# Kernel optimization log

Measured on AMD Instinct MI355X. Metric: run time of the kernel, lower is better.

Reference implementation:

```python
import jax
import jax.numpy as jnp
import numpy as np
from jax.scipy.linalg import expm

H = 2048   # hidden_size
R = 1      # low-rank dimension
B = 2048   # batch of independent (h, x) pairs


def _glorot(key, shape):
    return jax.random.uniform(key, shape, minval=-1.0, maxval=1.0) * jnp.sqrt(2.0 / sum(shape))


def setup_inputs() -> dict:
    key = jax.random.key(0)
    k1, k2, k3, k4, k5, k6 = jax.random.split(key, 6)
    return {
        "h": jax.random.normal(k5, (B, H), dtype=jnp.float32),
        "x": jax.random.normal(k6, (B, H), dtype=jnp.float32),
        # a_diag ~ U(-1, 0) * init_scale (10.0): negative real diagonal
        "a_diag": jax.random.uniform(k1, (H,), minval=-1.0, maxval=0.0) * 10.0,
        "p_vec": _glorot(k2, (H, R)),
        "q_vec": _glorot(k3, (H, R)),
        "b_mat": _glorot(k4, (H, H)),
        "delta": jnp.array(0.1, dtype=jnp.float32),
    }


def reference(h, x, a_diag, p_vec, q_vec, b_mat, delta):
    # A = diag(a_diag) + P Q^T  (DPLR structure, materialized dense as in source)
    A = jnp.diag(a_diag) + p_vec @ q_vec.T                       # [H, H]
    # Discretized state matrix: exp(delta * A)
    expA = expm(delta * A)                                       # [H, H]
    # Discretized input matrix: A^{-1} (exp(delta A) - I) B  (pinv as in source)
    A_inv = jnp.linalg.pinv(A)                                   # [H, H]
    B_disc = A_inv @ (expA - jnp.eye(H, dtype=A.dtype)) @ b_mat  # [H, H]
    # Batched recurrence step: A h + B x  for each row of h, x
    return h @ expA.T + x @ B_disc.T                             # [B, H]
```

## Files before the change

### kernel.cpp

```cpp
#include <hip/hip_runtime.h>

#define MAXM 16
#define NL_CAP 256
#define THETA 0.04f
#define SMEM_BYTES 36864

typedef unsigned short u16;
typedef u16 u16x8 __attribute__((ext_vector_type(8)));
typedef u16 u16x4 __attribute__((ext_vector_type(4)));
typedef __bf16 bf16x8 __attribute__((ext_vector_type(8)));
typedef float f32x4 __attribute__((ext_vector_type(4)));


__device__ __forceinline__ u16 f2bf(float f) {
    unsigned u = __float_as_uint(f);
    return (u16)((u + 0x7fffu + ((u >> 16) & 1u)) >> 16);
}

__global__ __launch_bounds__(256)
void conv_k(const float* __restrict__ x, const float* __restrict__ b,
            u16* __restrict__ xb, u16* __restrict__ bb, long nx, long nb)
{
    long i = ((long)blockIdx.x * 256 + threadIdx.x) * 4;
    if (i < nx) {
        float4 v = *(const float4*)&x[i];
        u16x4 o = {f2bf(v.x), f2bf(v.y), f2bf(v.z), f2bf(v.w)};
        *(u16x4*)&xb[i] = o;
    }
    if (i < nb) {
        float4 v = *(const float4*)&b[i];
        u16x4 o = {f2bf(v.x), f2bf(v.y), f2bf(v.z), f2bf(v.w)};
        *(u16x4*)&bb[i] = o;
    }
}


__device__ __forceinline__ double frcp(double den) {
    double r = (double)__builtin_amdgcn_rcpf((float)den);
    return fma(r, fma(-den, r, 1.0), r);
}


__device__ __forceinline__ void gload_lds16(const void* g, void* l) {
    __builtin_amdgcn_global_load_lds(
        (const __attribute__((address_space(1))) unsigned int*)g,
        (__attribute__((address_space(3))) unsigned int*)l, 16, 0, 0);
}

__device__ __forceinline__ void gemm_tile(u16* Al, u16* Bl, int tid, int bx, int by,
                                          const u16* __restrict__ A,
                                          const u16* __restrict__ B,
                                          float* __restrict__ C,
                                          int Ndim, int Kstride, int Klen)
{
    const int bm = by * 128, bn = bx * 128;
    const int wv = tid >> 6, ln = tid & 63;
    const int wr = (wv >> 1) * 64, wc = (wv & 1) * 64;
    const int fr = ln & 15, fk = (ln >> 4) * 8;

    const int r0 = tid >> 2, c0 = (tid & 3) * 8;
    const u16* Ap0 = A + (size_t)(bm + r0) * Kstride + c0;
    const u16* Ap1 = Ap0 + (size_t)64 * Kstride;
    const u16* Bp0 = B + (size_t)(bn + r0) * Kstride + c0;
    const u16* Bp1 = Bp0 + (size_t)64 * Kstride;
    u16* AlW0 = Al + wv * 512;
    u16* AlW1 = Al + 2048 + wv * 512;
    u16* BlW0 = Bl + wv * 512;
    u16* BlW1 = Bl + 2048 + wv * 512;

    f32x4 acc[4][4];
#pragma unroll
    for (int m = 0; m < 4; ++m)
#pragma unroll
        for (int n = 0; n < 4; ++n) acc[m][n] = (f32x4)0.f;

    for (int kk = 0; kk < Klen; kk += 32) {
        __syncthreads();
        gload_lds16(Ap0 + kk, AlW0);
        gload_lds16(Ap1 + kk, AlW1);
        gload_lds16(Bp0 + kk, BlW0);
        gload_lds16(Bp1 + kk, BlW1);
        __syncthreads();
        u16x8 af[4], bf[4];
#pragma unroll
        for (int m = 0; m < 4; ++m)
            af[m] = *(const u16x8*)&Al[(wr + m * 16 + fr) * 32 + fk];
#pragma unroll
        for (int n = 0; n < 4; ++n)
            bf[n] = *(const u16x8*)&Bl[(wc + n * 16 + fr) * 32 + fk];
#pragma unroll
        for (int m = 0; m < 4; ++m)
#pragma unroll
            for (int n = 0; n < 4; ++n)
                acc[m][n] = __builtin_amdgcn_mfma_f32_16x16x32_bf16(
                    __builtin_bit_cast(bf16x8, af[m]),
                    __builtin_bit_cast(bf16x8, bf[n]), acc[m][n], 0, 0, 0);
    }

    const int crow = (ln >> 4) * 4;
#pragma unroll
    for (int m = 0; m < 4; ++m)
#pragma unroll
        for (int n = 0; n < 4; ++n) {
            const size_t base = (size_t)(bm + wr + m * 16 + crow) * Ndim
                              + bn + wc + n * 16 + fr;
#pragma unroll
            for (int j = 0; j < 4; ++j)
                C[base + (size_t)j * Ndim] = acc[m][n][j];
        }
}

__global__ __launch_bounds__(256)
void bgemm_k(const u16* __restrict__ A, const u16* __restrict__ B,
             float* __restrict__ C, int Ndim, int Kdim)
{
    __shared__ __align__(16) unsigned char smem[SMEM_BYTES];
    gemm_tile((u16*)smem, (u16*)smem + 4096, threadIdx.x,
              blockIdx.x, blockIdx.y, A, B, C, Ndim, Kdim, Kdim);
}


__global__ __launch_bounds__(256)
void g_sgemm_k(const float* __restrict__ A, const float* __restrict__ B,
               float* __restrict__ C, int Mdim, int Ndim, int Kdim)
{
    __shared__ __align__(16) float As[16][132];
    __shared__ __align__(16) float Bs[16][68];
    const int tid = threadIdx.x;
    const int tx = tid & 15, ty = tid >> 4;
    const int bn = blockIdx.x * 64, bm = blockIdx.y * 128;
    const int lrA = tid >> 1, lcA = (tid & 1) << 3;
    const int lrB = tid >> 2, lcB = (tid & 3) << 2;
    const float* Aptr = A + (size_t)(bm + lrA) * Kdim + lcA;
    const float* Bptr = B + (size_t)(bn + lrB) * Kdim + lcB;
    float4 a0 = *(const float4*)(Aptr);
    float4 a1 = *(const float4*)(Aptr + 4);
    float4 b0 = *(const float4*)(Bptr);
    float acc[8][4];
#pragma unroll
    for (int i = 0; i < 8; ++i)
#pragma unroll
        for (int j = 0; j < 4; ++j) acc[i][j] = 0.f;
    for (int kk = 0; kk < Kdim; kk += 16) {
        __syncthreads();
        As[lcA + 0][lrA] = a0.x; As[lcA + 1][lrA] = a0.y;
        As[lcA + 2][lrA] = a0.z; As[lcA + 3][lrA] = a0.w;
        As[lcA + 4][lrA] = a1.x; As[lcA + 5][lrA] = a1.y;
        As[lcA + 6][lrA] = a1.z; As[lcA + 7][lrA] = a1.w;
        Bs[lcB + 0][lrB] = b0.x; Bs[lcB + 1][lrB] = b0.y;
        Bs[lcB + 2][lrB] = b0.z; Bs[lcB + 3][lrB] = b0.w;
        __syncthreads();
        if (kk + 16 < Kdim) {
            a0 = *(const float4*)(Aptr + kk + 16);
            a1 = *(const float4*)(Aptr + kk + 20);
            b0 = *(const float4*)(Bptr + kk + 16);
        }
#pragma unroll
        for (int k = 0; k < 16; ++k) {
            const float4 av0 = *(const float4*)&As[k][ty * 8];
            const float4 av1 = *(const float4*)&As[k][ty * 8 + 4];
            const float4 bv  = *(const float4*)&Bs[k][tx * 4];
            const float avf[8] = {av0.x, av0.y, av0.z, av0.w, av1.x, av1.y, av1.z, av1.w};
            const float bvf[4] = {bv.x, bv.y, bv.z, bv.w};
#pragma unroll
            for (int i = 0; i < 8; ++i)
#pragma unroll
                for (int j = 0; j < 4; ++j) acc[i][j] += avf[i] * bvf[j];
        }
    }
#pragma unroll
    for (int i = 0; i < 8; ++i) {
        const int r = bm + ty * 8 + i;
        float4 v = {acc[i][0], acc[i][1], acc[i][2], acc[i][3]};
        *(float4*)&C[(size_t)r * Ndim + bn + tx * 4] = v;
    }
}


__device__ __forceinline__ double wsum(double x) {
#pragma unroll
    for (int m = 32; m; m >>= 1) x += __shfl_xor(x, m, 64);
    return x;
}
__device__ __forceinline__ float wsumf(float x) {
#pragma unroll
    for (int m = 32; m; m >>= 1) x += __shfl_xor(x, m, 64);
    return x;
}

__device__ __forceinline__ int inert(double s11, double s12, double s22,
                                     double dc, double cS)
{
    double b00 = cS - s11, b01 = -1.0 - s12, b11 = -s22;
    double det = b00 * b11 - b01 * b01, tr = b00 + b11;
    int neg = (det > 0.0) ? ((tr < 0.0) ? 2 : 0) : 1;
    return (int)(dc + 0.5) + neg - 1;
}

__device__ __forceinline__ int lane_evalN32(float tf, double td, int n4,
    const float4* l0, const float4* l1, const float4* l2,
    const double* pc, bool poly, double cS,
    double& g11o, double& g12o, double& g22o)
{
    float s11 = 0.f, s12 = 0.f, s22 = 0.f, dc = 0.f;
#pragma unroll 2
    for (int i = 0; i < n4; ++i) {
        const float4 d4 = l0[i], x4 = l1[i], y4 = l2[i];
        const float dd[4] = {d4.x, d4.y, d4.z, d4.w};
        const float xx[4] = {x4.x, x4.y, x4.z, x4.w};
        const float yy[4] = {y4.x, y4.y, y4.z, y4.w};
#pragma unroll
        for (int e = 0; e < 4; ++e) {
            float den = dd[e] - tf;
            float mag = fmaxf(fabsf(den), 1e-30f);
            den = (den < 0.f) ? -mag : mag;
            const float inv = __builtin_amdgcn_rcpf(den);
            s11 = fmaf(xx[e] * xx[e], inv, s11);
            s12 = fmaf(xx[e] * yy[e], inv, s12);
            s22 = fmaf(yy[e] * yy[e], inv, s22);
            if (dd[e] < tf) dc += 1.f;
        }
    }
    double S11 = (double)s11, S12 = (double)s12, S22 = (double)s22;
    if (poly) {
        S11 += pc[0] + td * (pc[3] + td * (pc[6] + td * pc[9]));
        S12 += pc[1] + td * (pc[4] + td * (pc[7] + td * pc[10]));
        S22 += pc[2] + td * (pc[5] + td * (pc[8] + td * pc[11]));
    }
    g11o = S11; g12o = S12; g22o = S22;
    return inert(S11, S12, S22, (double)dc, cS);
}

__device__ void spec256(unsigned char* smem, int tid,
                        const float* __restrict__ av, const float* __restrict__ pv,
                        const float* __restrict__ qv, double* __restrict__ hdr,
                        float* __restrict__ V)
{
    __builtin_amdgcn_s_setprio(1);

    float* sd2 = (float*)smem;
    float* sw1 = sd2 + 2048;
    float* sw2 = sw1 + 2048;
    float* nl0 = sw2 + 2048;
    float* nl1 = nl0 + NL_CAP;
    float* nl2 = nl1 + NL_CAP;
    double* dsh = (double*)(nl2 + NL_CAP);
    int* ish = (int*)(dsh + 192);

    const int lane = tid & 63, wv = tid >> 6;
    const int j0 = tid * 8;

    float d2r[8], w1r[8], w2r[8];
    double cS = 0, n1 = 0, n2 = 0, mx = 0;
#pragma unroll
    for (int h = 0; h < 2; ++h) {
        float4 aa = *(const float4*)&av[j0 + h * 4];
        float4 pp = *(const float4*)&pv[j0 + h * 4];
        float4 qq = *(const float4*)&qv[j0 + h * 4];
        const float a4[4] = {aa.x, aa.y, aa.z, aa.w};
        const float p4[4] = {pp.x, pp.y, pp.z, pp.w};
        const float q4[4] = {qq.x, qq.y, qq.z, qq.w};
#pragma unroll
        for (int e = 0; e < 4; ++e) {
            const int ix = h * 4 + e;
            d2r[ix] = a4[e] * a4[e];
            w1r[ix] = a4[e] * p4[e];
            w2r[ix] = q4[e];
            sd2[j0 + ix] = d2r[ix]; sw1[j0 + ix] = w1r[ix]; sw2[j0 + ix] = w2r[ix];
            cS += (double)p4[e] * p4[e];
            n1 += (double)w1r[ix] * w1r[ix];
            n2 += (double)w2r[ix] * w2r[ix];
            mx = fmax(mx, (double)d2r[ix]);
        }
    }
    cS = wsum(cS); n1 = wsum(n1); n2 = wsum(n2);
#pragma unroll
    for (int m_ = 32; m_; m_ >>= 1) mx = fmax(mx, __shfl_xor(mx, m_, 64));
    __syncthreads();
    if (lane == 0) { dsh[wv] = cS; dsh[4 + wv] = n1; dsh[8 + wv] = n2; dsh[12 + wv] = mx; }
    __syncthreads();
    cS = 0; n1 = 0; n2 = 0; mx = 0;
    for (int w = 0; w < 4; ++w) {
        cS += dsh[w]; n1 += dsh[4 + w]; n2 += dsh[8 + w];
        mx = fmax(mx, dsh[12 + w]);
    }
    __syncthreads();

    double lo = 0.0;
    double hi = mx + 0.5 * (cS + sqrt(cS * cS + 4.0)) * (n1 + n2) + 1.0;
    for (int r = 0; r < 5; ++r) {
        const double td = lo + (hi - lo) * (double)(wv + 1) / 5.0;
        const float tf = (float)td;
        float s11 = 0.f, s12 = 0.f, s22 = 0.f, dc = 0.f;
        for (int i4 = lane; i4 < 512; i4 += 64) {
            const float4 dd = ((const float4*)sd2)[i4];
            const float4 e1 = ((const float4*)sw1)[i4];
            const float4 e2 = ((const float4*)sw2)[i4];
            const float df[4] = {dd.x, dd.y, dd.z, dd.w};
            const float f1[4] = {e1.x, e1.y, e1.z, e1.w};
            const float f2[4] = {e2.x, e2.y, e2.z, e2.w};
#pragma unroll
            for (int e = 0; e < 4; ++e) {
                float den = df[e] - tf;
                float mag = fmaxf(fabsf(den), 1e-30f);
                den = (den < 0.f) ? -mag : mag;
                const float inv = __builtin_amdgcn_rcpf(den);
                s11 = fmaf(f1[e] * f1[e], inv, s11);
                s12 = fmaf(f1[e] * f2[e], inv, s12);
                s22 = fmaf(f2[e] * f2[e], inv, s22);
                if (df[e] < tf) dc += 1.f;
            }
        }
        s11 = wsumf(s11); s12 = wsumf(s12); s22 = wsumf(s22); dc = wsumf(dc);
        if (lane == 0)
            ish[wv] = inert((double)s11, (double)s12, (double)s22, (double)dc, cS);
        __syncthreads();
        double nlo = lo, nhi = hi;
        for (int i = 0; i < 4; ++i) {
            double ti = lo + (hi - lo) * (double)(i + 1) / 5.0;
            if (ish[i] >= 2048) { if (ti < nhi) nhi = ti; }
            else                { if (ti > nlo) nlo = ti; }
        }
        lo = nlo; hi = nhi;
        __syncthreads();
    }
    const double lmax = 0.5 * (lo + hi);
    const double rc = 10.0 * 2048.0 * 1.1920928955078125e-07;
    const double cut2 = rc * rc * lmax;

    int flags = 0, lc = 0;
#pragma unroll
    for (int e = 0; e < 8; ++e)
        if (d2r[e] < THETA) { flags |= (1 << e); ++lc; }
    int sc = lc;
#pragma unroll
    for (int off = 1; off < 64; off <<= 1) {
        int y = __shfl_up(sc, off, 64);
        if (lane >= off) sc += y;
    }
    const int wtot = __shfl(sc, 63, 64);
    const int excl = sc - lc;
    if (lane == 0) ish[4 + wv] = wtot;
    __syncthreads();
    int base = excl;
    for (int w = 0; w < wv; ++w) base += ish[4 + w];
    int cnt = 0;
    for (int w = 0; w < 4; ++w) cnt += ish[4 + w];
    {
        int pos = base;
#pragma unroll
        for (int e = 0; e < 8; ++e) {
            if (flags & (1 << e)) {
                if (pos < NL_CAP) { nl0[pos] = d2r[e]; nl1[pos] = w1r[e]; nl2[pos] = w2r[e]; }
                ++pos;
            }
        }
    }
    const int cntPad = (cnt + 7) & ~7;
    if (tid == 0) {
        for (int i = cnt; i < cntPad && i < NL_CAP; ++i) {
            nl0[i] = 1e30f; nl1[i] = 0.f; nl2[i] = 0.f;
        }
        ish[8] = cnt; ish[10] = cntPad >> 2;
    }

    float cff[12];
#pragma unroll
    for (int c = 0; c < 12; ++c) cff[c] = 0.f;
#pragma unroll
    for (int e = 0; e < 8; ++e) {
        if (d2r[e] >= THETA) {
            float id = __builtin_amdgcn_rcpf(d2r[e]);
            float b1 = w1r[e], b2 = w2r[e];
            float x11 = b1 * b1, x12 = b1 * b2, x22 = b2 * b2;
            float f = id;
            cff[0] += x11 * f; cff[1]  += x12 * f; cff[2]  += x22 * f; f *= id;
            cff[3] += x11 * f; cff[4]  += x12 * f; cff[5]  += x22 * f; f *= id;
            cff[6] += x11 * f; cff[7]  += x12 * f; cff[8]  += x22 * f; f *= id;
            cff[9] += x11 * f; cff[10] += x12 * f; cff[11] += x22 * f;
        }
    }
#pragma unroll
    for (int c = 0; c < 12; ++c) cff[c] = wsumf(cff[c]);
    if (lane == 0) {
        double* dw = &dsh[16 + wv * 12];
#pragma unroll
        for (int c = 0; c < 12; ++c) dw[c] = (double)cff[c];
    }
    __syncthreads();
    if (tid < 12) {
        double s = 0;
        for (int w = 0; w < 4; ++w) s += dsh[16 + w * 12 + tid];
        dsh[96 + tid] = s;
    }
    __syncthreads();

    cnt = ish[8];
    const bool nearOK = (cnt <= NL_CAP - 8);
    const float4* l0 = nearOK ? (const float4*)nl0 : (const float4*)sd2;
    const float4* l1 = nearOK ? (const float4*)nl1 : (const float4*)sw1;
    const float4* l2 = nearOK ? (const float4*)nl2 : (const float4*)sw2;
    const int n4 = nearOK ? ish[10] : 512;
    const bool poly = nearOK;
    const double* pcoef = &dsh[96];

    double zg1, zg2, zg3;
    if (wv == 0) {
        int N = lane_evalN32((float)cut2, cut2, n4, l0, l1, l2, pcoef, poly, cS,
                             zg1, zg2, zg3);
        if (lane == 0) ish[9] = N;
    }
    __syncthreads();
    int m = ish[9];
    if (m < 0) m = 0;
    if (m > MAXM) m = MAXM;

    for (int k = wv; k < m; k += 4) {
        double klo = 0.0, khi = cut2;
        for (int r = 0; r < 3; ++r) {
            const double w = khi - klo;
            const double td = klo + w * (double)(lane + 1) / 65.0;
            int N = lane_evalN32((float)td, td, n4, l0, l1, l2, pcoef, poly, cS,
                                 zg1, zg2, zg3);
            unsigned long long mask = __ballot(N >= k + 1);
            int j = (mask == 0ull) ? 64 : (__ffsll(mask) - 1);
            double nk = (j == 64) ? khi : (klo + w * (double)(j + 1) / 65.0);
            klo = klo + w * (double)j / 65.0;
            khi = nk;
        }
        const double lam = 0.5 * (klo + khi);
        double g11, g12, g22;
        lane_evalN32((float)lam, lam, n4, l0, l1, l2, pcoef, poly, cS, g11, g12, g22);
        const double m00 = 1.0 + g12, m01 = g11 + cS * g12;
        const double m10 = g22,       m11 = 1.0 + g12 + cS * g22;
        double y1, y2;
        if (m00 * m00 + m01 * m01 >= m10 * m10 + m11 * m11) { y1 = m01; y2 = -m00; }
        else                                                { y1 = m11; y2 = -m10; }
        if (lane == 0) {
            dsh[112 + 3 * k]     = lam;
            dsh[112 + 3 * k + 1] = y2;
            dsh[112 + 3 * k + 2] = y1 + cS * y2;
        }
    }
    __syncthreads();

    for (int k = 0; k < m; ++k) {
        const double lam = dsh[112 + 3 * k];
        const double z1 = dsh[112 + 3 * k + 1], z2 = dsh[112 + 3 * k + 2];
        double vr[8], pn = 0;
#pragma unroll
        for (int e = 0; e < 8; ++e) {
            double den = (double)d2r[e] - lam;
            if (fabs(den) < 1e-25) den = (den < 0 ? -1e-25 : 1e-25);
            vr[e] = ((double)w1r[e] * z1 + (double)w2r[e] * z2) * frcp(den);
            pn += vr[e] * vr[e];
        }
        pn = wsum(pn);
        if (lane == 0) dsh[160 + wv] = pn;
        __syncthreads();
        double tot = 0;
        for (int w = 0; w < 4; ++w) tot += dsh[160 + w];
        const double inv = 1.0 / sqrt(tot);
        float o0[8];
#pragma unroll
        for (int e = 0; e < 8; ++e) o0[e] = (float)(vr[e] * inv);
        *(float4*)&V[(size_t)k * 2048 + j0]     = *(float4*)&o0[0];
        *(float4*)&V[(size_t)k * 2048 + j0 + 4] = *(float4*)&o0[4];
        __syncthreads();
    }

    if (tid == 0) { hdr[0] = lmax; hdr[1] = cut2; hdr[2] = (double)m; hdr[3] = cS; }
    __builtin_amdgcn_s_setprio(0);
}


__global__ __launch_bounds__(256)
void fat_k(const u16* __restrict__ A, const u16* __restrict__ B,
           float* __restrict__ C0, float* __restrict__ C1,
           int Ndim, int Kdim, int ntiles, int nbx, int nsplit,
           const float* __restrict__ av, const float* __restrict__ pv,
           const float* __restrict__ qv, double* __restrict__ hdr,
           float* __restrict__ V)
{
    __shared__ __align__(16) unsigned char smem[SMEM_BYTES];
    const int bid = blockIdx.x;
    if (bid == 0) {
        spec256(smem, threadIdx.x, av, pv, qv, hdr, V);
        return;
    }
    const int t = bid - 1;
    if (t >= ntiles * nsplit) return;
    const int ks = t / ntiles;
    const int tt = t - ks * ntiles;
    const int Klen = Kdim / nsplit;
    gemm_tile((u16*)smem, (u16*)smem + 4096, threadIdx.x,
              tt % nbx, tt / nbx,
              A + (size_t)ks * Klen, B + (size_t)ks * Klen,
              ks ? C1 : C0, Ndim, Kdim, Klen);
}


__global__ __launch_bounds__(256, 2)
void series_k(float* __restrict__ io, const float* __restrict__ io2, int addP,
              const float* __restrict__ hm,
              const float* __restrict__ qv, const float* __restrict__ pv,
              const float* __restrict__ av, const float* __restrict__ delta,
              const float* __restrict__ V, const double* __restrict__ hdr,
              int useTrunc)
{
    const int lane = threadIdx.x & 63;
    const int row = blockIdx.x * 4 + (threadIdx.x >> 6);
    const float d = delta[0];
    const int m = useTrunc ? (int)hdr[2] : 0;

    float q[32], p[32], a[32], t[32], o[32];
    float* iorow = io + (size_t)row * 2048;
    const float* io2row = io2 + (size_t)row * 2048;
#pragma unroll
    for (int cc = 0; cc < 8; ++cc) {
        const int j = cc * 256 + lane * 4;
        *(float4*)&q[cc * 4] = *(const float4*)&qv[j];
        *(float4*)&p[cc * 4] = *(const float4*)&pv[j];
        *(float4*)&a[cc * 4] = *(const float4*)&av[j];
        float4 u0 = *(const float4*)&iorow[j];
        if (addP) {
            const float4 u1 = *(const float4*)&io2row[j];
            u0.x += u1.x; u0.y += u1.y; u0.z += u1.z; u0.w += u1.w;
        }
        *(float4*)&t[cc * 4] = u0;
    }
#pragma unroll
    for (int e = 0; e < 32; ++e) o[e] = t[e];

    float cf = 1.f;
    for (int k = 1; k <= 13; ++k) {
        float s = 0.f;
#pragma unroll
        for (int e = 0; e < 32; ++e) s += t[e] * q[e];
#pragma unroll
        for (int msk = 32; msk; msk >>= 1) s += __shfl_xor(s, msk, 64);
        cf /= (float)(k + 1);
        const float ds = d * s;
#pragma unroll
        for (int e = 0; e < 32; ++e) { t[e] = d * a[e] * t[e] + ds * p[e]; o[e] += cf * t[e]; }
    }
#pragma unroll
    for (int e = 0; e < 32; ++e) o[e] *= d;

    for (int k = 0; k < m; ++k) {
        const float* vr = V + (size_t)k * 2048;
        float vk[32];
#pragma unroll
        for (int cc = 0; cc < 8; ++cc)
            *(float4*)&vk[cc * 4] = *(const float4*)&vr[cc * 256 + lane * 4];
        float s = 0.f;
#pragma unroll
        for (int e = 0; e < 32; ++e) s += o[e] * vk[e];
#pragma unroll
        for (int msk = 32; msk; msk >>= 1) s += __shfl_xor(s, msk, 64);
#pragma unroll
        for (int e = 0; e < 32; ++e) o[e] -= s * vk[e];
    }

    const float* hrow = hm + (size_t)row * 2048;
#pragma unroll
    for (int cc = 0; cc < 8; ++cc)
        *(float4*)&t[cc * 4] = *(const float4*)&hrow[cc * 256 + lane * 4];
#pragma unroll
    for (int e = 0; e < 32; ++e) o[e] += t[e];
    cf = 1.f;
    for (int k = 1; k <= 14; ++k) {
        float s = 0.f;
#pragma unroll
        for (int e = 0; e < 32; ++e) s += t[e] * q[e];
#pragma unroll
        for (int msk = 32; msk; msk >>= 1) s += __shfl_xor(s, msk, 64);
        cf /= (float)k;
        const float ds = d * s;
#pragma unroll
        for (int e = 0; e < 32; ++e) { t[e] = d * a[e] * t[e] + ds * p[e]; o[e] += cf * t[e]; }
    }
#pragma unroll
    for (int cc = 0; cc < 8; ++cc)
        *(float4*)&iorow[cc * 256 + lane * 4] = *(const float4*)&o[cc * 4];
}


extern "C" void kernel_launch(void* const* d_in, const int* in_sizes, int n_in,
                              void* d_out, int out_size, void* d_ws, size_t ws_size,
                              hipStream_t stream)
{
    const float* hmat  = (const float*)d_in[0];
    const float* xmat  = (const float*)d_in[1];
    const float* adiag = (const float*)d_in[2];
    const float* pvec  = (const float*)d_in[3];
    const float* qvec  = (const float*)d_in[4];
    const float* bmat  = (const float*)d_in[5];
    const float* delta = (const float*)d_in[6];
    float* out = (float*)d_out;

    const int H  = in_sizes[2];
    const int Bb = in_sizes[0] / H;
    const size_t SZ = (size_t)Bb * H;
    const size_t HH = (size_t)H * H;

    double* hdr = (double*)d_ws;
    float* V = (float*)(hdr + 8);
    u16* xb = (u16*)(V + (size_t)MAXM * H);
    u16* bb = xb + SZ;
    float* C1 = (float*)(bb + HH);

    const size_t needSpec  = 64 + (size_t)MAXM * H * sizeof(float);
    const size_t needFull  = needSpec + (SZ + HH) * sizeof(u16);
    const size_t needSplit = needFull + SZ * sizeof(float);
    const bool doTrunc = (H == 2048) && (ws_size >= needSpec);
    const bool doBf16  = (ws_size >= needFull) && (H % 128 == 0) && (Bb % 128 == 0);
    const bool doSplit = doBf16 && doTrunc && (ws_size >= needSplit) && (H % 64 == 0);

    dim3 blk256(256);
    const int nbx = H / 128;
    const int ntiles = nbx * (Bb / 128);

    if (doBf16) {
        const long nmax = (long)(SZ > HH ? SZ : HH);
        const int cg = (int)((nmax / 4 + 255) / 256);
        conv_k<<<cg, blk256, 0, stream>>>(xmat, bmat, xb, bb, (long)SZ, (long)HH);
        if (doTrunc) {
            const int nsplit = doSplit ? 2 : 1;
            fat_k<<<1 + ntiles * nsplit, blk256, 0, stream>>>(
                xb, bb, out, C1, H, H, ntiles, nbx, nsplit,
                adiag, pvec, qvec, hdr, V);
        } else {
            dim3 gg(nbx, Bb / 128);
            bgemm_k<<<gg, blk256, 0, stream>>>(xb, bb, out, H, H);
        }
    } else {
        if (doTrunc)
            fat_k<<<1, blk256, 0, stream>>>(nullptr, nullptr, out, nullptr,
                                            H, H, 0, 1, 1,
                                            adiag, pvec, qvec, hdr, V);
        dim3 gg(H / 64, Bb / 128);
        g_sgemm_k<<<gg, blk256, 0, stream>>>(xmat, bmat, out, Bb, H, H);
    }

    series_k<<<Bb / 4, blk256, 0, stream>>>(out, doSplit ? C1 : out,
                                            doSplit ? 1 : 0,
                                            hmat, qvec, pvec, adiag, delta,
                                            V, hdr, doTrunc ? 1 : 0);
}
```

Measured before the change: 91.41 us.

## Double-buffer LDS tiles in bf16 GEMM to overlap global loads with MFMA

The bf16 GEMM tile loop now keeps two LDS buffers for the A and B tiles. It issues the global-to-LDS loads for the next K-slice before computing on the current one, and uses a partial vmcnt wait so only the current slice's loads must finish. The goal is to hide global memory latency behind MFMA work instead of stalling on two barriers every iteration. LDS use per tile doubles (the B buffer offset moves to 8192 elements), and a wrong wait count or buffer aliasing with the spec256 path sharing smem could cause races.

```diff
diff --git a/kernel.cpp b/kernel.cpp
--- a/kernel.cpp
+++ b/kernel.cpp
@@ -3,7 +3,7 @@
 #define MAXM 16
 #define NL_CAP 256
 #define THETA 0.04f
-#define SMEM_BYTES 36864
+#define SMEM_BYTES 32768
 
 typedef unsigned short u16;
 typedef u16 u16x8 __attribute__((ext_vector_type(8)));
@@ -63,10 +63,6 @@
     const u16* Ap1 = Ap0 + (size_t)64 * Kstride;
     const u16* Bp0 = B + (size_t)(bn + r0) * Kstride + c0;
     const u16* Bp1 = Bp0 + (size_t)64 * Kstride;
-    u16* AlW0 = Al + wv * 512;
-    u16* AlW1 = Al + 2048 + wv * 512;
-    u16* BlW0 = Bl + wv * 512;
-    u16* BlW1 = Bl + 2048 + wv * 512;
 
     f32x4 acc[4][4];
 #pragma unroll
@@ -74,20 +70,45 @@
 #pragma unroll
         for (int n = 0; n < 4; ++n) acc[m][n] = (f32x4)0.f;
 
+    {
+        u16* a0 = Al + wv * 512;
+        u16* a1 = Al + 2048 + wv * 512;
+        u16* b0 = Bl + wv * 512;
+        u16* b1 = Bl + 2048 + wv * 512;
+        gload_lds16(Ap0, a0);
+        gload_lds16(Ap1, a1);
+        gload_lds16(Bp0, b0);
+        gload_lds16(Bp1, b1);
+    }
+
+    int cur = 0;
     for (int kk = 0; kk < Klen; kk += 32) {
-        __syncthreads();
-        gload_lds16(Ap0 + kk, AlW0);
-        gload_lds16(Ap1 + kk, AlW1);
-        gload_lds16(Bp0 + kk, BlW0);
-        gload_lds16(Bp1 + kk, BlW1);
-        __syncthreads();
+        const bool hasNext = (kk + 32 < Klen);
+        if (hasNext) {
+            const int nb = (cur ^ 1) * 4096;
+            u16* a0 = Al + nb + wv * 512;
+            u16* a1 = Al + nb + 2048 + wv * 512;
+            u16* b0 = Bl + nb + wv * 512;
+            u16* b1 = Bl + nb + 2048 + wv * 512;
+            gload_lds16(Ap0 + kk + 32, a0);
+            gload_lds16(Ap1 + kk + 32, a1);
+            gload_lds16(Bp0 + kk + 32, b0);
+            gload_lds16(Bp1 + kk + 32, b1);
+            asm volatile("s_waitcnt vmcnt(4)" ::: "memory");
+        } else {
+            asm volatile("s_waitcnt vmcnt(0)" ::: "memory");
+        }
+        __builtin_amdgcn_sched_barrier(0);
+        __builtin_amdgcn_s_barrier();
+
+        const int cb = cur * 4096;
         u16x8 af[4], bf[4];
 #pragma unroll
         for (int m = 0; m < 4; ++m)
-            af[m] = *(const u16x8*)&Al[(wr + m * 16 + fr) * 32 + fk];
+            af[m] = *(const u16x8*)&Al[cb + (wr + m * 16 + fr) * 32 + fk];
 #pragma unroll
         for (int n = 0; n < 4; ++n)
-            bf[n] = *(const u16x8*)&Bl[(wc + n * 16 + fr) * 32 + fk];
+            bf[n] = *(const u16x8*)&Bl[cb + (wc + n * 16 + fr) * 32 + fk];
 #pragma unroll
         for (int m = 0; m < 4; ++m)
 #pragma unroll
@@ -95,6 +116,10 @@
                 acc[m][n] = __builtin_amdgcn_mfma_f32_16x16x32_bf16(
                     __builtin_bit_cast(bf16x8, af[m]),
                     __builtin_bit_cast(bf16x8, bf[n]), acc[m][n], 0, 0, 0);
+
+        __builtin_amdgcn_sched_barrier(0);
+        __builtin_amdgcn_s_barrier();
+        cur ^= 1;
     }
 
     const int crow = (ln >> 4) * 4;
@@ -115,7 +140,7 @@
              float* __restrict__ C, int Ndim, int Kdim)
 {
     __shared__ __align__(16) unsigned char smem[SMEM_BYTES];
-    gemm_tile((u16*)smem, (u16*)smem + 4096, threadIdx.x,
+    gemm_tile((u16*)smem, (u16*)smem + 8192, threadIdx.x,
               blockIdx.x, blockIdx.y, A, B, C, Ndim, Kdim, Kdim);
 }
 
@@ -493,7 +518,7 @@
     const int ks = t / ntiles;
     const int tt = t - ks * ntiles;
     const int Klen = Kdim / nsplit;
-    gemm_tile((u16*)smem, (u16*)smem + 4096, threadIdx.x,
+    gemm_tile((u16*)smem, (u16*)smem + 8192, threadIdx.x,
               tt % nbx, tt / nbx,
               A + (size_t)ks * Klen, B + (size_t)ks * Klen,
               ks ? C1 : C0, Ndim, Kdim, Klen);
```

Result: faster. 84.91 us (-7.1%).
